# Kernel tuning notes

Measured on AMD Instinct MI355X. Metric: run time of the kernel, lower is better.

Reference implementation:

```python
import jax, jax.numpy as jnp
import numpy as np

B, H, W, C_IN, C_OUT, KH, KW = 32, 56, 56, 128, 256, 3, 3


def setup_inputs() -> dict:
    key = jax.random.key(0)
    k1, k2, k3 = jax.random.split(key, 3)
    x = jax.random.normal(k1, (B, H, W, C_IN), dtype=jnp.float32)
    w = jax.random.normal(k2, (KH, KW, C_IN, C_OUT), dtype=jnp.float32) * 0.05
    b = jax.random.normal(k3, (C_OUT,), dtype=jnp.float32) * 0.05
    return {"x": x, "w": w, "b": b}


def reference(x, w, b):
    # SAME-padded, stride-1 2D conv (math identical to the im2col loop in the
    # original, collapsed into a single conv/GEMM) plus bias.
    out = jax.lax.conv_general_dilated(
        x, w,
        window_strides=(1, 1),
        padding="SAME",
        dimension_numbers=("NHWC", "HWIO", "NHWC"),
    )
    return out + b
```

## Files before the change

kernel.cpp:

```cpp
#include <hip/hip_runtime.h>

#define B_ 32
#define CI 128
#define CO 256
#define K_DIM 1152
#define M_DIM 100352
#define BM 128
#define BN 128
#define KT 18
#define HPAD 58
#define XB_OFF 589824
#define WTBLK 72
#define XPBLK 6728
#define GRID_M 784

typedef float          floatx4  __attribute__((ext_vector_type(4)));
typedef unsigned short ushortx8 __attribute__((ext_vector_type(8)));
typedef __bf16         bf16x8   __attribute__((ext_vector_type(8)));

typedef __attribute__((address_space(1))) void gas_void;
typedef __attribute__((address_space(3))) void las_void;
#define GLD16(g, l) __builtin_amdgcn_global_load_lds( \
    (gas_void*)(uintptr_t)(g), (las_void*)(l), 16, 0, 0)

__device__ __forceinline__ unsigned short bf16_rne(float f) {
    unsigned u = __builtin_bit_cast(unsigned, f);
    u += 0x7FFFu + ((u >> 16) & 1u);
    return (unsigned short)(u >> 16);
}

__global__ void prepass_kernel(const float* __restrict__ x,
                               const float* __restrict__ w,
                               unsigned short* __restrict__ xb,
                               unsigned short* __restrict__ wt) {
    __shared__ unsigned short tile[64][65];
    if (blockIdx.x < WTBLK) {
        const int kt = (blockIdx.x % 18) * 64, nt = (blockIdx.x / 18) * 64;
        #pragma unroll
        for (int i = 0; i < 16; ++i) {
            int idx = i * 256 + threadIdx.x;
            int kl = idx >> 6, nl = idx & 63;
            tile[kl][nl] = bf16_rne(w[(size_t)(kt + kl) * CO + nt + nl]);
        }
        __syncthreads();
        #pragma unroll
        for (int i = 0; i < 16; ++i) {
            int idx = i * 256 + threadIdx.x;
            int nl = idx >> 6, kl = idx & 63;
            wt[(size_t)(nt + nl) * K_DIM + kt + kl] = tile[kl][nl];
        }
    } else {
        const int t   = (blockIdx.x - WTBLK) * 256 + threadIdx.x;
        const int pix = t >> 4;
        const int cc  = (t & 15) << 3;
        const int b   = pix / (HPAD * HPAD);
        const int rem = pix % (HPAD * HPAD);
        const int hp  = rem / HPAD, wp = rem % HPAD;
        ushortx8 g = {0, 0, 0, 0, 0, 0, 0, 0};
        if (hp >= 1 && hp <= 56 && wp >= 1 && wp <= 56) {
            const float* s = x + ((size_t)((b * 56 + hp - 1) * 56 + (wp - 1))) * CI + cc;
            floatx4 f0 = ((const floatx4*)s)[0];
            floatx4 f1 = ((const floatx4*)s)[1];
            #pragma unroll
            for (int e = 0; e < 4; ++e) { g[e] = bf16_rne(f0[e]); g[e + 4] = bf16_rne(f1[e]); }
        }
        *(ushortx8*)(xb + (size_t)pix * CI + cc) = g;
    }
}

__global__ __launch_bounds__(256, 4)
void conv_gemm_kernel(const unsigned short* __restrict__ xb,
                      const unsigned short* __restrict__ wt,
                      const float* __restrict__ bias,
                      float* __restrict__ out) {
    __shared__ unsigned short As[2][BM * 32];
    __shared__ unsigned short Bs[2][BN * 32];

    const int tid  = threadIdx.x;
    const int bx   = blockIdx.y;
    const int bid  = blockIdx.x;
    const int by   = (bid & 7) * (GRID_M / 8) + (bid >> 3);
    const int wid  = tid >> 6;
    const int lane = tid & 63;
    const int lrow = lane & 15;
    const int quad = lane >> 4;
    const int wm   = (wid & 1) * 64;
    const int wn   = (wid >> 1) * 64;

    const int rseg = lane >> 2;
    const int cglb = ((lane & 3) - (rseg >> 1)) & 3;

    const unsigned short* aga[2];
    const unsigned short* bga[2];
    #pragma unroll
    for (int g = 0; g < 2; ++g) {
        const int m0 = by * BM + g * 64 + wid * 16 + rseg;
        const int b0 = m0 / 3136, r0 = m0 % 3136;
        aga[g] = xb + ((size_t)((b0 * HPAD + r0 / 56) * HPAD + r0 % 56)) * CI + cglb * 8;
        const int n0 = bx * BN + g * 64 + wid * 16 + rseg;
        bga[g] = wt + (size_t)n0 * K_DIM + cglb * 8;
    }
    const int wb0 = (wid * 16) * 32;
    const int wb1 = (64 + wid * 16) * 32;

    const int swz = ((quad + (lrow >> 1)) & 3) * 8;
    int arow[4], brow[4];
    #pragma unroll
    for (int i = 0; i < 4; ++i) {
        arow[i] = (wm + i * 16 + lrow) * 32 + swz;
        brow[i] = (wn + i * 16 + lrow) * 32 + swz;
    }

    floatx4 acc[4][4] = {};

    auto stageA = [&](int u, int kk) {
        const int p    = u >> 2;
        const int aoff = (p / 3 * HPAD + p % 3) * CI + (u & 3) * 32;
        GLD16(aga[0] + aoff, &As[kk][wb0]);
        GLD16(aga[1] + aoff, &As[kk][wb1]);
    };
    auto stageB = [&](int u, int kk) {
        const int boff = u * 32;
        GLD16(bga[0] + boff, &Bs[kk][wb0]);
        GLD16(bga[1] + boff, &Bs[kk][wb1]);
    };

    ushortx8 bfr[4], afr[4];
    auto compute = [&](int kk) {
        #pragma unroll
        for (int ni = 0; ni < 4; ++ni) bfr[ni] = *(const ushortx8*)&Bs[kk][brow[ni]];
        #pragma unroll
        for (int i = 0; i < 4; ++i) afr[i] = *(const ushortx8*)&As[kk][arow[i]];
        #pragma unroll
        for (int i = 0; i < 4; ++i)
            #pragma unroll
            for (int ni = 0; ni < 4; ++ni)
                acc[i][ni] = __builtin_amdgcn_mfma_f32_16x16x32_bf16(
                    __builtin_bit_cast(bf16x8, afr[i]),
                    __builtin_bit_cast(bf16x8, bfr[ni]),
                    acc[i][ni], 0, 0, 0);
    };

    #pragma unroll 1
    for (int t = 0; t < KT; ++t) {
        const int u = t * 2;
        stageA(u, 0); stageB(u, 0);
        stageA(u + 1, 1); stageB(u + 1, 1);
        __syncthreads();
        compute(0);
        compute(1);
        __syncthreads();
    }

    float bv[4];
    #pragma unroll
    for (int ni = 0; ni < 4; ++ni)
        bv[ni] = bias[bx * BN + wn + ni * 16 + lrow];

    #pragma unroll
    for (int mi = 0; mi < 4; ++mi) {
        #pragma unroll
        for (int r = 0; r < 4; ++r) {
            const int row = by * BM + wm + mi * 16 + quad * 4 + r;
            float* o = out + (size_t)row * CO + bx * BN + wn + lrow;
            #pragma unroll
            for (int ni = 0; ni < 4; ++ni)
                o[ni * 16] = acc[mi][ni][r] + bv[ni];
        }
    }
}

extern "C" void kernel_launch(void* const* d_in, const int* in_sizes, int n_in,
                              void* d_out, int out_size, void* d_ws, size_t ws_size,
                              hipStream_t stream) {
    (void)in_sizes; (void)n_in; (void)out_size; (void)ws_size;
    const float* x    = (const float*)d_in[0];
    const float* w    = (const float*)d_in[1];
    const float* bias = (const float*)d_in[2];
    float* out = (float*)d_out;

    unsigned short* wt = (unsigned short*)d_ws;
    unsigned short* xb = (unsigned short*)((char*)d_ws + XB_OFF);

    prepass_kernel<<<dim3(WTBLK + XPBLK), dim3(256), 0, stream>>>(x, w, xb, wt);
    conv_gemm_kernel<<<dim3(GRID_M, CO / BN), dim3(256), 0, stream>>>(xb, wt, bias, out);
}
```

Measured before the change: 203.9 us.

## Enlarge conv GEMM tile to 256x256 with 512 threads and double-buffered prefetch

Doubles the block tile to 256x256 so each block covers all output channels, using 8 waves of 512 threads with 8x4 MFMA tiles per wave. This raises operand reuse and halves the number of times A is read. The K loop also becomes a software-pipelined double buffer: the next slot is staged while the current one is computed, with one barrier per slot. In exchange it needs more accumulator registers and shared memory per block, and the grid is smaller, which lowers occupancy and may leave CUs unevenly loaded.

```diff
diff --git a/kernel.cpp b/kernel.cpp
--- a/kernel.cpp
+++ b/kernel.cpp
@@ -5,14 +5,14 @@
 #define CO 256
 #define K_DIM 1152
 #define M_DIM 100352
-#define BM 128
-#define BN 128
-#define KT 18
+#define BM 256
+#define BN 256
+#define NSLOT 36
 #define HPAD 58
 #define XB_OFF 589824
 #define WTBLK 72
 #define XPBLK 6728
-#define GRID_M 784
+#define GRID_M 392
 
 typedef float          floatx4  __attribute__((ext_vector_type(4)));
 typedef unsigned short ushortx8 __attribute__((ext_vector_type(8)));
@@ -68,7 +68,7 @@
     }
 }
 
-__global__ __launch_bounds__(256, 4)
+__global__ __launch_bounds__(512, 2)
 void conv_gemm_kernel(const unsigned short* __restrict__ xb,
                       const unsigned short* __restrict__ wt,
                       const float* __restrict__ bias,
@@ -77,14 +77,13 @@
     __shared__ unsigned short Bs[2][BN * 32];
 
     const int tid  = threadIdx.x;
-    const int bx   = blockIdx.y;
     const int bid  = blockIdx.x;
     const int by   = (bid & 7) * (GRID_M / 8) + (bid >> 3);
     const int wid  = tid >> 6;
     const int lane = tid & 63;
     const int lrow = lane & 15;
     const int quad = lane >> 4;
-    const int wm   = (wid & 1) * 64;
+    const int wm   = (wid & 1) * 128;
     const int wn   = (wid >> 1) * 64;
 
     const int rseg = lane >> 2;
@@ -94,45 +93,43 @@
     const unsigned short* bga[2];
     #pragma unroll
     for (int g = 0; g < 2; ++g) {
-        const int m0 = by * BM + g * 64 + wid * 16 + rseg;
+        const int m0 = by * BM + g * 128 + wid * 16 + rseg;
         const int b0 = m0 / 3136, r0 = m0 % 3136;
         aga[g] = xb + ((size_t)((b0 * HPAD + r0 / 56) * HPAD + r0 % 56)) * CI + cglb * 8;
-        const int n0 = bx * BN + g * 64 + wid * 16 + rseg;
+        const int n0 = g * 128 + wid * 16 + rseg;
         bga[g] = wt + (size_t)n0 * K_DIM + cglb * 8;
     }
-    const int wb0 = (wid * 16) * 32;
-    const int wb1 = (64 + wid * 16) * 32;
+    const int wbase = wid * 512;
 
     const int swz = ((quad + (lrow >> 1)) & 3) * 8;
-    int arow[4], brow[4];
+    int arow[8], brow[4];
     #pragma unroll
-    for (int i = 0; i < 4; ++i) {
-        arow[i] = (wm + i * 16 + lrow) * 32 + swz;
-        brow[i] = (wn + i * 16 + lrow) * 32 + swz;
-    }
+    for (int i = 0; i < 8; ++i) arow[i] = (wm + i * 16 + lrow) * 32 + swz;
+    #pragma unroll
+    for (int i = 0; i < 4; ++i) brow[i] = (wn + i * 16 + lrow) * 32 + swz;
 
-    floatx4 acc[4][4] = {};
+    floatx4 acc[8][4] = {};
 
-    auto stageA = [&](int u, int kk) {
+    auto stageA = [&](int u, int P) {
         const int p    = u >> 2;
         const int aoff = (p / 3 * HPAD + p % 3) * CI + (u & 3) * 32;
-        GLD16(aga[0] + aoff, &As[kk][wb0]);
-        GLD16(aga[1] + aoff, &As[kk][wb1]);
+        GLD16(aga[0] + aoff, &As[P][wbase]);
+        GLD16(aga[1] + aoff, &As[P][4096 + wbase]);
     };
-    auto stageB = [&](int u, int kk) {
+    auto stageB = [&](int u, int P) {
         const int boff = u * 32;
-        GLD16(bga[0] + boff, &Bs[kk][wb0]);
-        GLD16(bga[1] + boff, &Bs[kk][wb1]);
+        GLD16(bga[0] + boff, &Bs[P][wbase]);
+        GLD16(bga[1] + boff, &Bs[P][4096 + wbase]);
     };
 
-    ushortx8 bfr[4], afr[4];
-    auto compute = [&](int kk) {
+    auto compute = [&](int P) {
+        ushortx8 bfr[4], afr[8];
         #pragma unroll
-        for (int ni = 0; ni < 4; ++ni) bfr[ni] = *(const ushortx8*)&Bs[kk][brow[ni]];
+        for (int ni = 0; ni < 4; ++ni) bfr[ni] = *(const ushortx8*)&Bs[P][brow[ni]];
         #pragma unroll
-        for (int i = 0; i < 4; ++i) afr[i] = *(const ushortx8*)&As[kk][arow[i]];
+        for (int i = 0; i < 8; ++i) afr[i] = *(const ushortx8*)&As[P][arow[i]];
         #pragma unroll
-        for (int i = 0; i < 4; ++i)
+        for (int i = 0; i < 8; ++i)
             #pragma unroll
             for (int ni = 0; ni < 4; ++ni)
                 acc[i][ni] = __builtin_amdgcn_mfma_f32_16x16x32_bf16(
@@ -141,28 +138,29 @@
                     acc[i][ni], 0, 0, 0);
     };
 
+    stageA(0, 0); stageB(0, 0);
+    __syncthreads();
     #pragma unroll 1
-    for (int t = 0; t < KT; ++t) {
-        const int u = t * 2;
-        stageA(u, 0); stageB(u, 0);
-        stageA(u + 1, 1); stageB(u + 1, 1);
-        __syncthreads();
-        compute(0);
-        compute(1);
+    for (int u = 0; u < NSLOT - 1; ++u) {
+        const int b = u & 1;
+        stageA(u + 1, b ^ 1);
+        stageB(u + 1, b ^ 1);
+        compute(b);
         __syncthreads();
     }
+    compute(1);
 
     float bv[4];
     #pragma unroll
     for (int ni = 0; ni < 4; ++ni)
-        bv[ni] = bias[bx * BN + wn + ni * 16 + lrow];
+        bv[ni] = bias[wn + ni * 16 + lrow];
 
     #pragma unroll
-    for (int mi = 0; mi < 4; ++mi) {
+    for (int mi = 0; mi < 8; ++mi) {
         #pragma unroll
         for (int r = 0; r < 4; ++r) {
             const int row = by * BM + wm + mi * 16 + quad * 4 + r;
-            float* o = out + (size_t)row * CO + bx * BN + wn + lrow;
+            float* o = out + (size_t)row * CO + wn + lrow;
             #pragma unroll
             for (int ni = 0; ni < 4; ++ni)
                 o[ni * 16] = acc[mi][ni][r] + bv[ni];
@@ -183,5 +181,5 @@
     unsigned short* xb = (unsigned short*)((char*)d_ws + XB_OFF);
 
     prepass_kernel<<<dim3(WTBLK + XPBLK), dim3(256), 0, stream>>>(x, w, xb, wt);
-    conv_gemm_kernel<<<dim3(GRID_M, CO / BN), dim3(256), 0, stream>>>(xb, wt, bias, out);
+    conv_gemm_kernel<<<dim3(GRID_M), dim3(512), 0, stream>>>(xb, wt, bias, out);
 }
```

Measured after the change: 237.5 us. 1.16x slower.

## Widen GEMM block tile to cover all 256 output channels

Applied to the files above, without the earlier changes.

Each block now computes a 128x256 output tile, so every activation tile is loaded from global memory once instead of twice across the two N blocks, and the grid collapses to one dimension. Each wave accumulates a 64x128 sub-tile (32 MFMA accumulators), which raises register use and halves the target occupancy in launch bounds. Shared memory for B doubles, and the grid shrinks to 784 blocks.

```diff
diff --git a/kernel.cpp b/kernel.cpp
--- a/kernel.cpp
+++ b/kernel.cpp
@@ -6,7 +6,7 @@
 #define K_DIM 1152
 #define M_DIM 100352
 #define BM 128
-#define BN 128
+#define BN 256
 #define KT 18
 #define HPAD 58
 #define XB_OFF 589824
@@ -68,7 +68,7 @@
     }
 }
 
-__global__ __launch_bounds__(256, 4)
+__global__ __launch_bounds__(256, 2)
 void conv_gemm_kernel(const unsigned short* __restrict__ xb,
                       const unsigned short* __restrict__ wt,
                       const float* __restrict__ bias,
@@ -77,7 +77,6 @@
     __shared__ unsigned short Bs[2][BN * 32];
 
     const int tid  = threadIdx.x;
-    const int bx   = blockIdx.y;
     const int bid  = blockIdx.x;
     const int by   = (bid & 7) * (GRID_M / 8) + (bid >> 3);
     const int wid  = tid >> 6;
@@ -85,56 +84,59 @@
     const int lrow = lane & 15;
     const int quad = lane >> 4;
     const int wm   = (wid & 1) * 64;
-    const int wn   = (wid >> 1) * 64;
+    const int wn   = (wid >> 1) * 128;
 
     const int rseg = lane >> 2;
     const int cglb = ((lane & 3) - (rseg >> 1)) & 3;
 
     const unsigned short* aga[2];
-    const unsigned short* bga[2];
+    const unsigned short* bga[4];
     #pragma unroll
     for (int g = 0; g < 2; ++g) {
         const int m0 = by * BM + g * 64 + wid * 16 + rseg;
         const int b0 = m0 / 3136, r0 = m0 % 3136;
         aga[g] = xb + ((size_t)((b0 * HPAD + r0 / 56) * HPAD + r0 % 56)) * CI + cglb * 8;
-        const int n0 = bx * BN + g * 64 + wid * 16 + rseg;
+    }
+    #pragma unroll
+    for (int g = 0; g < 4; ++g) {
+        const int n0 = g * 64 + wid * 16 + rseg;
         bga[g] = wt + (size_t)n0 * K_DIM + cglb * 8;
     }
-    const int wb0 = (wid * 16) * 32;
-    const int wb1 = (64 + wid * 16) * 32;
+    const int wbase = wid * 512;
 
     const int swz = ((quad + (lrow >> 1)) & 3) * 8;
-    int arow[4], brow[4];
+    int arow[4], brow[8];
     #pragma unroll
-    for (int i = 0; i < 4; ++i) {
-        arow[i] = (wm + i * 16 + lrow) * 32 + swz;
-        brow[i] = (wn + i * 16 + lrow) * 32 + swz;
-    }
+    for (int i = 0; i < 4; ++i) arow[i] = (wm + i * 16 + lrow) * 32 + swz;
+    #pragma unroll
+    for (int i = 0; i < 8; ++i) brow[i] = (wn + i * 16 + lrow) * 32 + swz;
 
-    floatx4 acc[4][4] = {};
+    floatx4 acc[4][8] = {};
 
-    auto stageA = [&](int u, int kk) {
+    auto stageA = [&](int u) {
         const int p    = u >> 2;
         const int aoff = (p / 3 * HPAD + p % 3) * CI + (u & 3) * 32;
-        GLD16(aga[0] + aoff, &As[kk][wb0]);
-        GLD16(aga[1] + aoff, &As[kk][wb1]);
+        GLD16(aga[0] + aoff, &As[u & 1][wbase]);
+        GLD16(aga[1] + aoff, &As[u & 1][2048 + wbase]);
     };
-    auto stageB = [&](int u, int kk) {
+    auto stageB = [&](int u) {
         const int boff = u * 32;
-        GLD16(bga[0] + boff, &Bs[kk][wb0]);
-        GLD16(bga[1] + boff, &Bs[kk][wb1]);
+        GLD16(bga[0] + boff, &Bs[u & 1][wbase]);
+        GLD16(bga[1] + boff, &Bs[u & 1][2048 + wbase]);
+        GLD16(bga[2] + boff, &Bs[u & 1][4096 + wbase]);
+        GLD16(bga[3] + boff, &Bs[u & 1][6144 + wbase]);
     };
 
-    ushortx8 bfr[4], afr[4];
     auto compute = [&](int kk) {
-        #pragma unroll
-        for (int ni = 0; ni < 4; ++ni) bfr[ni] = *(const ushortx8*)&Bs[kk][brow[ni]];
+        ushortx8 afr[4], bfr[8];
         #pragma unroll
         for (int i = 0; i < 4; ++i) afr[i] = *(const ushortx8*)&As[kk][arow[i]];
         #pragma unroll
+        for (int ni = 0; ni < 8; ++ni) bfr[ni] = *(const ushortx8*)&Bs[kk][brow[ni]];
+        #pragma unroll
         for (int i = 0; i < 4; ++i)
             #pragma unroll
-            for (int ni = 0; ni < 4; ++ni)
+            for (int ni = 0; ni < 8; ++ni)
                 acc[i][ni] = __builtin_amdgcn_mfma_f32_16x16x32_bf16(
                     __builtin_bit_cast(bf16x8, afr[i]),
                     __builtin_bit_cast(bf16x8, bfr[ni]),
@@ -144,27 +146,27 @@
     #pragma unroll 1
     for (int t = 0; t < KT; ++t) {
         const int u = t * 2;
-        stageA(u, 0); stageB(u, 0);
-        stageA(u + 1, 1); stageB(u + 1, 1);
+        stageA(u);     stageB(u);
+        stageA(u + 1); stageB(u + 1);
         __syncthreads();
         compute(0);
         compute(1);
         __syncthreads();
     }
 
-    float bv[4];
+    float bv[8];
     #pragma unroll
-    for (int ni = 0; ni < 4; ++ni)
-        bv[ni] = bias[bx * BN + wn + ni * 16 + lrow];
+    for (int ni = 0; ni < 8; ++ni)
+        bv[ni] = bias[wn + ni * 16 + lrow];
 
     #pragma unroll
     for (int mi = 0; mi < 4; ++mi) {
         #pragma unroll
         for (int r = 0; r < 4; ++r) {
             const int row = by * BM + wm + mi * 16 + quad * 4 + r;
-            float* o = out + (size_t)row * CO + bx * BN + wn + lrow;
+            float* o = out + (size_t)row * CO + wn + lrow;
             #pragma unroll
-            for (int ni = 0; ni < 4; ++ni)
+            for (int ni = 0; ni < 8; ++ni)
                 o[ni * 16] = acc[mi][ni][r] + bv[ni];
         }
     }
@@ -183,5 +185,5 @@
     unsigned short* xb = (unsigned short*)((char*)d_ws + XB_OFF);
 
     prepass_kernel<<<dim3(WTBLK + XPBLK), dim3(256), 0, stream>>>(x, w, xb, wt);
-    conv_gemm_kernel<<<dim3(GRID_M, CO / BN), dim3(256), 0, stream>>>(xb, wt, bias, out);
+    conv_gemm_kernel<<<dim3(GRID_M), dim3(256), 0, stream>>>(xb, wt, bias, out);
 }
```

New measurement: 209.5 us. 1.03x slower.
